# Kernel tuning notes

Hardware: AMD Instinct MI355X
Metric: run time of the kernel (lower is better)

## Reference

```python
import jax, jax.numpy as jnp
import numpy as np

NEG_SLOPE = 0.2


def _gat_layer(x, src, dst, W, a_src, a_dst, b, concat):
    """PyG-style GATConv (with self-loops already appended to src/dst).
    x: [N, Fin], W: [Fin, H*D], a_src/a_dst: [H, D], b: [H*D] or [D].
    """
    N = x.shape[0]
    H, D = a_src.shape
    h = (x @ W).reshape(N, H, D)                      # per-head projections
    es = jnp.einsum('nhd,hd->nh', h, a_src)           # alpha_src per node
    ed = jnp.einsum('nhd,hd->nh', h, a_dst)           # alpha_dst per node
    e = jax.nn.leaky_relu(es[src] + ed[dst], NEG_SLOPE)   # [E, H] edge logits
    # segment softmax over incoming edges of each target node
    m = jax.ops.segment_max(e, dst, num_segments=N)       # [N, H]
    ex = jnp.exp(e - m[dst])
    s = jax.ops.segment_sum(ex, dst, num_segments=N)      # [N, H]
    alpha = ex / jnp.where(s > 0, s, 1.0)[dst]            # [E, H]
    out = jax.ops.segment_sum(h[src] * alpha[:, :, None], dst, num_segments=N)  # [N,H,D]
    out = out.reshape(N, H * D) if concat else out.mean(axis=1)
    return out + b


def setup_inputs() -> dict:
    key = jax.random.key(0)
    ks = jax.random.split(key, 16)
    N, E, F_IN, HID, HEADS, NG, NC = 50000, 1000000, 128, 64, 4, 512, 2
    x = jax.random.normal(ks[0], (N, F_IN), dtype=jnp.float32)
    edge_index = jax.random.randint(ks[1], (2, E), 0, N, dtype=jnp.int32)
    batch = jnp.sort(jax.random.randint(ks[2], (N,), 0, NG, dtype=jnp.int32))
    sc = 0.1
    params = {
        'W1': jax.random.normal(ks[3], (F_IN, HEADS * HID), dtype=jnp.float32) * sc,
        'a_src1': jax.random.normal(ks[4], (HEADS, HID), dtype=jnp.float32) * sc,
        'a_dst1': jax.random.normal(ks[5], (HEADS, HID), dtype=jnp.float32) * sc,
        'b1': jnp.zeros((HEADS * HID,), dtype=jnp.float32),
        'W2': jax.random.normal(ks[6], (HEADS * HID, HID), dtype=jnp.float32) * sc,
        'a_src2': jax.random.normal(ks[7], (1, HID), dtype=jnp.float32) * sc,
        'a_dst2': jax.random.normal(ks[8], (1, HID), dtype=jnp.float32) * sc,
        'b2': jnp.zeros((HID,), dtype=jnp.float32),
        'Wc': jax.random.normal(ks[9], (HID, NC), dtype=jnp.float32) * sc,
        'bc': jnp.zeros((NC,), dtype=jnp.float32),
    }
    return {'x': x, 'edge_index': edge_index, 'batch': batch, 'num_graphs': NG, **params}


def reference(x, edge_index, batch, num_graphs, W1, a_src1, a_dst1, b1,
              W2, a_src2, a_dst2, b2, Wc, bc):
    N = x.shape[0]
    # PyG GATConv adds self-loops by default
    loops = jnp.arange(N, dtype=edge_index.dtype)
    src = jnp.concatenate([edge_index[0], loops])
    dst = jnp.concatenate([edge_index[1], loops])
    h = jax.nn.elu(_gat_layer(x, src, dst, W1, a_src1, a_dst1, b1, concat=True))
    h = jax.nn.elu(_gat_layer(h, src, dst, W2, a_src2, a_dst2, b2, concat=False))
    # global mean pool per graph
    sums = jax.ops.segment_sum(h, batch, num_segments=num_graphs)         # [G, HID]
    cnt = jax.ops.segment_sum(jnp.ones((N,), h.dtype), batch, num_segments=num_graphs)
    pooled = sums / jnp.maximum(cnt, 1.0)[:, None]
    return pooled @ Wc + bc
```

## Files before the change

kernel.cpp:

```cpp
#include <hip/hip_runtime.h>

#define NN   50000
#define NE   1000000
#define FIN  128
#define HID  64
#define HEADS 4
#define C1   256
#define NG   512
#define ETOT (NE + NN)
#define BSH  10
#define NBUK 49
#define CHUNK 8192
#define NCHUNK 123
#define NPREP 192
#define NHIST 64

typedef __attribute__((ext_vector_type(8))) short bf16x8;
typedef __attribute__((ext_vector_type(4))) short bf16x4;
typedef __attribute__((ext_vector_type(4))) float f32x4;
typedef __attribute__((ext_vector_type(2))) float f32x2;

__device__ __forceinline__ float lrelu(float v) { return v > 0.f ? v : 0.2f * v; }
__device__ __forceinline__ float eluf(float v)  { return v > 0.f ? v : __expf(v) - 1.f; }

__device__ __forceinline__ unsigned short f2bf(float f) {
    unsigned u = __float_as_uint(f);
    unsigned r = (u + 0x7FFFu + ((u >> 16) & 1u)) >> 16;
    return (unsigned short)r;
}
__device__ __forceinline__ float bf2f(unsigned short b) {
    return __uint_as_float(((unsigned)b) << 16);
}
__device__ __forceinline__ unsigned char f2fp8(float f) {
    int w = __builtin_amdgcn_cvt_pk_fp8_f32(f, f, 0, false);
    return (unsigned char)(w & 0xFF);
}

__global__ __launch_bounds__(256) void k_setup(const float* __restrict__ W1,
                                               const float* __restrict__ W2,
                                               const int* __restrict__ dst,
                                               const int* __restrict__ batch,
                                               unsigned short* __restrict__ W1t,
                                               unsigned short* __restrict__ W2t,
                                               int* __restrict__ bhist,
                                               int* __restrict__ gstart) {
    int b = blockIdx.x;
    int tid = threadIdx.x;
    if (b < NPREP) {
        int i = b * 256 + tid;
        if (i < FIN * C1) {
            int k = i / C1, c = i % C1;
            W1t[c * FIN + k] = f2bf(W1[i]);
        } else {
            int j = i - FIN * C1;
            if (j < C1 * HID) {
                int k = j / HID, c = j % HID;
                W2t[c * C1 + k] = f2bf(W2[j]);
            }
        }
    } else if (b < NPREP + NHIST) {
        __shared__ int lh[NBUK];
        if (tid < NBUK) lh[tid] = 0;
        __syncthreads();
        for (int e = (b - NPREP) * 256 + tid; e < NE; e += NHIST * 256)
            atomicAdd(&lh[dst[e] >> BSH], 1);
        __syncthreads();
        if (tid < NBUK) atomicAdd(&bhist[tid], lh[tid]);
    } else {
        for (int g = tid; g <= NG; g += 256) {
            int lo = 0, hi = NN;
            while (lo < hi) {
                int mid = (lo + hi) >> 1;
                if (batch[mid] < g) lo = mid + 1; else hi = mid;
            }
            gstart[g] = lo;
        }
    }
}

__global__ void k_bscan(const int* __restrict__ bhist,
                        int* __restrict__ bbase,
                        int* __restrict__ bcur,
                        int* __restrict__ offs) {
    int tid = threadIdx.x;
    int v = (tid < NBUK) ? bhist[tid] : 0;
    int x = v;
    #pragma unroll
    for (int off = 1; off < 64; off <<= 1) {
        int t = __shfl_up(x, off);
        if (tid >= off) x += t;
    }
    if (tid < NBUK) {
        int excl = x - v;
        bbase[tid] = excl;
        bcur[tid] = excl;
    }
    if (tid == NBUK - 1) bbase[NBUK] = x;
    if (tid == 0) offs[NN] = ETOT;
}

__global__ __launch_bounds__(256) void k_part(const int* __restrict__ src,
                                              const int* __restrict__ dst,
                                              int* __restrict__ bcur,
                                              int2* __restrict__ ebuf) {
    __shared__ int lcnt[NBUK];
    __shared__ int gbase[NBUK];
    __shared__ int lrank[NBUK];
    int tid = threadIdx.x;
    int e0 = blockIdx.x * CHUNK;
    int e1 = min(e0 + CHUNK, NE);
    if (tid < NBUK) { lcnt[tid] = 0; lrank[tid] = 0; }
    __syncthreads();
    for (int e = e0 + tid; e < e1; e += 256)
        atomicAdd(&lcnt[dst[e] >> BSH], 1);
    __syncthreads();
    if (tid < NBUK) gbase[tid] = atomicAdd(&bcur[tid], lcnt[tid]);
    __syncthreads();
    for (int e = e0 + tid; e < e1; e += 256) {
        int d = dst[e];
        int b = d >> BSH;
        int r = atomicAdd(&lrank[b], 1);
        ebuf[gbase[b] + r] = make_int2(src[e], d);
    }
}

__global__ __launch_bounds__(1024) void k_bfill(const int2* __restrict__ ebuf,
                                                const int* __restrict__ bbase,
                                                int* __restrict__ offs,
                                                int* __restrict__ colsrc) {
    __shared__ int ldeg[1024];
    __shared__ int lcur[1024];
    __shared__ int ws[16];
    int b = blockIdx.x;
    int tid = threadIdx.x;
    int nbase = b << BSH;
    int ncnt = min(1024, NN - nbase);
    int ebeg = bbase[b], eend = bbase[b + 1];
    ldeg[tid] = 0;
    __syncthreads();
    for (int i = ebeg + tid; i < eend; i += 1024)
        atomicAdd(&ldeg[ebuf[i].y - nbase], 1);
    __syncthreads();
    int v = (tid < ncnt) ? ldeg[tid] + 1 : 0;
    int lane = tid & 63, wv = tid >> 6;
    int x = v;
    #pragma unroll
    for (int off = 1; off < 64; off <<= 1) {
        int t = __shfl_up(x, off);
        if (lane >= off) x += t;
    }
    if (lane == 63) ws[wv] = x;
    __syncthreads();
    if (tid < 16) {
        int y = ws[tid];
        #pragma unroll
        for (int off = 1; off < 16; off <<= 1) {
            int t = __shfl_up(y, off);
            if (tid >= off) y += t;
        }
        ws[tid] = y;
    }
    __syncthreads();
    int base = wv ? ws[wv - 1] : 0;
    int excl = base + x - v;
    int gofs = ebeg + nbase + excl;
    if (tid < ncnt) {
        offs[nbase + tid] = gofs;
        lcur[tid] = gofs;
    }
    __syncthreads();
    for (int i = ebeg + tid; i < eend; i += 1024) {
        int2 ed = ebuf[i];
        int p = atomicAdd(&lcur[ed.y - nbase], 1);
        colsrc[p] = ed.x;
    }
    __syncthreads();
    if (tid < ncnt) colsrc[lcur[tid]] = nbase + tid;
}

__global__ __launch_bounds__(256) void k_gemm1(const float* __restrict__ x,
                                               const unsigned short* __restrict__ W1t,
                                               const float* __restrict__ asrc,
                                               const float* __restrict__ adst,
                                               unsigned char* __restrict__ h1f,
                                               float* __restrict__ es1,
                                               float* __restrict__ ed1) {
    __shared__ unsigned short Wl[128 * FIN];
    int tid = threadIdx.x;
    int lane = tid & 63, wv = tid >> 6;
    int r0 = (blockIdx.x * 4 + wv) * 16;
    int g = lane >> 4, q = lane & 15;

    int ar = min(r0 + q, NN - 1);
    const float* xr = x + (size_t)ar * FIN;
    bf16x8 afr[4];
    #pragma unroll
    for (int kt = 0; kt < 4; ++kt) {
        float4 u0 = *(const float4*)(xr + kt * 32 + g * 8);
        float4 u1 = *(const float4*)(xr + kt * 32 + g * 8 + 4);
        bf16x8 a;
        a[0] = (short)f2bf(u0.x); a[1] = (short)f2bf(u0.y);
        a[2] = (short)f2bf(u0.z); a[3] = (short)f2bf(u0.w);
        a[4] = (short)f2bf(u1.x); a[5] = (short)f2bf(u1.y);
        a[6] = (short)f2bf(u1.z); a[7] = (short)f2bf(u1.w);
        afr[kt] = a;
    }

    for (int ch = 0; ch < 2; ++ch) {
        if (ch) __syncthreads();
        const uint4* src = (const uint4*)(W1t + (size_t)ch * 128 * FIN);
        #pragma unroll
        for (int i = 0; i < 8; ++i) {
            int idx = tid + i * 256;
            uint4 v = src[idx];
            unsigned byte = (unsigned)idx << 4;
            unsigned dst = byte ^ (((byte >> 8) & 7) << 4);
            *(uint4*)((char*)Wl + dst) = v;
        }
        __syncthreads();

        #pragma unroll
        for (int hh = 0; hh < 2; ++hh) {
            int h = ch * 2 + hh;
            float ps[4] = {0.f, 0.f, 0.f, 0.f};
            float pd[4] = {0.f, 0.f, 0.f, 0.f};
            #pragma unroll
            for (int tl = 0; tl < 4; ++tl) {
                int col = (h * 4 + tl) * 16 + q;
                int cl = col - ch * 128;
                f32x4 acc = {0.f, 0.f, 0.f, 0.f};
                #pragma unroll
                for (int kt = 0; kt < 4; ++kt) {
                    unsigned bb = (unsigned)cl * 256 + kt * 64 + g * 16;
                    bf16x8 b = *(const bf16x8*)((const char*)Wl + (bb ^ (((unsigned)cl & 7) << 4)));
                    acc = __builtin_amdgcn_mfma_f32_16x16x32_bf16(afr[kt], b, acc, 0, 0, 0);
                }
                float av = asrc[col], bv = adst[col];
                #pragma unroll
                for (int j = 0; j < 4; ++j) {
                    int rr = min(r0 + g * 4 + j, NN - 1);
                    h1f[(size_t)rr * C1 + col] = f2fp8(acc[j]);
                    ps[j] += acc[j] * av;
                    pd[j] += acc[j] * bv;
                }
            }
            #pragma unroll
            for (int j = 0; j < 4; ++j) {
                #pragma unroll
                for (int off = 1; off < 16; off <<= 1) {
                    ps[j] += __shfl_xor(ps[j], off);
                    pd[j] += __shfl_xor(pd[j], off);
                }
                if (q == 0) {
                    int rr = min(r0 + g * 4 + j, NN - 1);
                    es1[rr * 4 + h] = ps[j];
                    ed1[rr * 4 + h] = pd[j];
                }
            }
        }
    }
}

__global__ __launch_bounds__(512) void k_agg1(const int* __restrict__ offs,
                                              const int* __restrict__ colsrc,
                                              const unsigned char* __restrict__ h1f,
                                              const float* __restrict__ es1,
                                              const float* __restrict__ ed1,
                                              const float* __restrict__ b1,
                                              unsigned short* __restrict__ h1p) {
    __shared__ int   sls[8][64];
    __shared__ float sla[8][64][4];
    int lane = threadIdx.x & 63, wv = threadIdx.x >> 6;
    int n = blockIdx.x * 8 + wv;
    if (n >= NN) return;
    int beg = offs[n], end = offs[n + 1], deg = end - beg;
    float4 edv = *(const float4*)(ed1 + n * 4);
    int half = lane >> 5, q5 = lane & 31;
    int hd = q5 >> 3;
    f32x2 acc2[4];
    #pragma unroll
    for (int j = 0; j < 4; ++j) acc2[j] = (f32x2){0.f, 0.f};

    if (deg <= 64) {
        int msrc = 0;
        float m0 = 0.f, m1 = 0.f, m2 = 0.f, m3 = 0.f;
        if (lane < deg) {
            msrc = colsrc[beg + lane];
            float4 ev = *(const float4*)(es1 + msrc * 4);
            m0 = __expf(lrelu(ev.x + edv.x));
            m1 = __expf(lrelu(ev.y + edv.y));
            m2 = __expf(lrelu(ev.z + edv.z));
            m3 = __expf(lrelu(ev.w + edv.w));
        }
        float s0 = m0, s1 = m1, s2 = m2, s3 = m3;
        #pragma unroll
        for (int off = 1; off < 64; off <<= 1) {
            s0 += __shfl_xor(s0, off);
            s1 += __shfl_xor(s1, off);
            s2 += __shfl_xor(s2, off);
            s3 += __shfl_xor(s3, off);
        }
        sls[wv][lane] = msrc;
        sla[wv][lane][0] = m0 * (1.f / s0);
        sla[wv][lane][1] = m1 * (1.f / s1);
        sla[wv][lane][2] = m2 * (1.f / s2);
        sla[wv][lane][3] = m3 * (1.f / s3);

        for (int i = 0; i < deg; i += 16) {
            uint2 hv[8];
            float a[8];
            #pragma unroll
            for (int u = 0; u < 8; ++u) {
                int ee = (i + 2 * u + half) & 63;
                int s = sls[wv][ee];
                a[u] = sla[wv][ee][hd];
                hv[u] = *(const uint2*)(h1f + (size_t)s * C1 + q5 * 8);
            }
            #pragma unroll
            for (int u = 0; u < 8; ++u) {
                f32x2 av = (f32x2){a[u], a[u]};
                f32x2 p;
                p = __builtin_amdgcn_cvt_pk_f32_fp8(hv[u].x, false); acc2[0] += p * av;
                p = __builtin_amdgcn_cvt_pk_f32_fp8(hv[u].x, true);  acc2[1] += p * av;
                p = __builtin_amdgcn_cvt_pk_f32_fp8(hv[u].y, false); acc2[2] += p * av;
                p = __builtin_amdgcn_cvt_pk_f32_fp8(hv[u].y, true);  acc2[3] += p * av;
            }
        }
    } else {
        float s0 = 0.f, s1 = 0.f, s2 = 0.f, s3 = 0.f;
        for (int i = beg + lane; i < end; i += 64) {
            int s = colsrc[i];
            float4 ev = *(const float4*)(es1 + s * 4);
            s0 += __expf(lrelu(ev.x + edv.x));
            s1 += __expf(lrelu(ev.y + edv.y));
            s2 += __expf(lrelu(ev.z + edv.z));
            s3 += __expf(lrelu(ev.w + edv.w));
        }
        #pragma unroll
        for (int off = 1; off < 64; off <<= 1) {
            s0 += __shfl_xor(s0, off);
            s1 += __shfl_xor(s1, off);
            s2 += __shfl_xor(s2, off);
            s3 += __shfl_xor(s3, off);
        }
        float rr = hd == 0 ? 1.f / s0 : hd == 1 ? 1.f / s1 : hd == 2 ? 1.f / s2 : 1.f / s3;
        float ed_h = hd == 0 ? edv.x : hd == 1 ? edv.y : hd == 2 ? edv.z : edv.w;
        for (int i = beg; i < end; i += 2) {
            int idx = i + half;
            if (idx < end) {
                int s = colsrc[idx];
                float eh = es1[s * 4 + hd] + ed_h;
                float av = __expf(lrelu(eh)) * rr;
                f32x2 a = (f32x2){av, av};
                uint2 hv = *(const uint2*)(h1f + (size_t)s * C1 + q5 * 8);
                f32x2 p;
                p = __builtin_amdgcn_cvt_pk_f32_fp8(hv.x, false); acc2[0] += p * a;
                p = __builtin_amdgcn_cvt_pk_f32_fp8(hv.x, true);  acc2[1] += p * a;
                p = __builtin_amdgcn_cvt_pk_f32_fp8(hv.y, false); acc2[2] += p * a;
                p = __builtin_amdgcn_cvt_pk_f32_fp8(hv.y, true);  acc2[3] += p * a;
            }
        }
    }

    float acc[8];
    #pragma unroll
    for (int j = 0; j < 4; ++j) { acc[2*j] = acc2[j][0]; acc[2*j+1] = acc2[j][1]; }
    #pragma unroll
    for (int j = 0; j < 8; ++j) acc[j] += __shfl_xor(acc[j], 32);

    if (half == 0) {
        float4 bv0 = *(const float4*)(b1 + q5 * 8);
        float4 bv1 = *(const float4*)(b1 + q5 * 8 + 4);
        bf16x8 o;
        o[0] = (short)f2bf(eluf(acc[0] + bv0.x));
        o[1] = (short)f2bf(eluf(acc[1] + bv0.y));
        o[2] = (short)f2bf(eluf(acc[2] + bv0.z));
        o[3] = (short)f2bf(eluf(acc[3] + bv0.w));
        o[4] = (short)f2bf(eluf(acc[4] + bv1.x));
        o[5] = (short)f2bf(eluf(acc[5] + bv1.y));
        o[6] = (short)f2bf(eluf(acc[6] + bv1.z));
        o[7] = (short)f2bf(eluf(acc[7] + bv1.w));
        *(bf16x8*)(h1p + (size_t)n * C1 + q5 * 8) = o;
    }
}

__global__ __launch_bounds__(256) void k_gemm2(const unsigned short* __restrict__ h1p,
                                               const unsigned short* __restrict__ W2t,
                                               const float* __restrict__ as2,
                                               const float* __restrict__ ad2,
                                               unsigned char* __restrict__ h2f,
                                               float* __restrict__ es2,
                                               float* __restrict__ ed2) {
    __shared__ unsigned short Wl[HID * C1];
    int tid = threadIdx.x;
    int lane = tid & 63, wv = tid >> 6;
    int r0 = (blockIdx.x * 4 + wv) * 16;
    int g = lane >> 4, q = lane & 15;

    const uint4* src = (const uint4*)W2t;
    #pragma unroll
    for (int i = 0; i < 8; ++i) {
        int idx = tid + i * 256;
        uint4 v = src[idx];
        unsigned byte = (unsigned)idx << 4;
        unsigned dst = byte ^ (((byte >> 9) & 7) << 4);
        *(uint4*)((char*)Wl + dst) = v;
    }

    int ar = min(r0 + q, NN - 1);
    const unsigned short* arp = h1p + (size_t)ar * C1;
    bf16x8 afr[8];
    #pragma unroll
    for (int kt = 0; kt < 8; ++kt)
        afr[kt] = *(const bf16x8*)(arp + kt * 32 + g * 8);

    __syncthreads();

    float ps[4] = {0.f, 0.f, 0.f, 0.f};
    float pd[4] = {0.f, 0.f, 0.f, 0.f};
    #pragma unroll
    for (int t = 0; t < 4; ++t) {
        int col = t * 16 + q;
        f32x4 acc = {0.f, 0.f, 0.f, 0.f};
        #pragma unroll
        for (int kt = 0; kt < 8; ++kt) {
            unsigned bb = (unsigned)col * 512 + kt * 64 + g * 16;
            bf16x8 b = *(const bf16x8*)((const char*)Wl + (bb ^ (((unsigned)col & 7) << 4)));
            acc = __builtin_amdgcn_mfma_f32_16x16x32_bf16(afr[kt], b, acc, 0, 0, 0);
        }
        float av = as2[col], bv = ad2[col];
        #pragma unroll
        for (int j = 0; j < 4; ++j) {
            int rr = min(r0 + g * 4 + j, NN - 1);
            h2f[(size_t)rr * HID + col] = f2fp8(acc[j]);
            ps[j] += acc[j] * av;
            pd[j] += acc[j] * bv;
        }
    }
    #pragma unroll
    for (int j = 0; j < 4; ++j) {
        #pragma unroll
        for (int off = 1; off < 16; off <<= 1) {
            ps[j] += __shfl_xor(ps[j], off);
            pd[j] += __shfl_xor(pd[j], off);
        }
        if (q == 0) {
            int rr = min(r0 + g * 4 + j, NN - 1);
            es2[rr] = ps[j];
            ed2[rr] = pd[j];
        }
    }
}

__global__ __launch_bounds__(512) void k_agg2(const int* __restrict__ offs,
                                              const int* __restrict__ colsrc,
                                              const unsigned char* __restrict__ h2f,
                                              const float* __restrict__ es2,
                                              const float* __restrict__ ed2,
                                              const float* __restrict__ b2,
                                              float* __restrict__ h3) {
    __shared__ int   sls[8][64];
    __shared__ float sla[8][64];
    int lane = threadIdx.x & 63, wv = threadIdx.x >> 6;
    int n = blockIdx.x * 8 + wv;
    if (n >= NN) return;
    int beg = offs[n], end = offs[n + 1], deg = end - beg;
    float edv = ed2[n];
    int g = lane >> 4, q = lane & 15;
    f32x2 acc2[2];
    acc2[0] = (f32x2){0.f, 0.f};
    acc2[1] = (f32x2){0.f, 0.f};

    if (deg <= 64) {
        int msrc = 0;
        float mex = 0.f;
        if (lane < deg) {
            msrc = colsrc[beg + lane];
            mex = __expf(lrelu(es2[msrc] + edv));
        }
        float ss = mex;
        #pragma unroll
        for (int off = 1; off < 64; off <<= 1) ss += __shfl_xor(ss, off);
        sls[wv][lane] = msrc;
        sla[wv][lane] = mex * (1.f / ss);

        for (int i = 0; i < deg; i += 32) {
            unsigned w[8];
            float a[8];
            #pragma unroll
            for (int u = 0; u < 8; ++u) {
                int ee = (i + 4 * u + g) & 63;
                int s = sls[wv][ee];
                a[u] = sla[wv][ee];
                w[u] = *(const unsigned*)(h2f + (size_t)s * HID + q * 4);
            }
            #pragma unroll
            for (int u = 0; u < 8; ++u) {
                f32x2 av = (f32x2){a[u], a[u]};
                f32x2 p;
                p = __builtin_amdgcn_cvt_pk_f32_fp8(w[u], false); acc2[0] += p * av;
                p = __builtin_amdgcn_cvt_pk_f32_fp8(w[u], true);  acc2[1] += p * av;
            }
        }
    } else {
        float ss = 0.f;
        for (int i = beg + lane; i < end; i += 64) {
            int s = colsrc[i];
            ss += __expf(lrelu(es2[s] + edv));
        }
        #pragma unroll
        for (int off = 1; off < 64; off <<= 1) ss += __shfl_xor(ss, off);
        float rs = 1.f / ss;
        for (int i = beg; i < end; i += 4) {
            int idx = i + g;
            if (idx < end) {
                int s = colsrc[idx];
                float av = __expf(lrelu(es2[s] + edv)) * rs;
                f32x2 a = (f32x2){av, av};
                unsigned w = *(const unsigned*)(h2f + (size_t)s * HID + q * 4);
                f32x2 p;
                p = __builtin_amdgcn_cvt_pk_f32_fp8(w, false); acc2[0] += p * a;
                p = __builtin_amdgcn_cvt_pk_f32_fp8(w, true);  acc2[1] += p * a;
            }
        }
    }

    float acc[4] = {acc2[0][0], acc2[0][1], acc2[1][0], acc2[1][1]};
    #pragma unroll
    for (int j = 0; j < 4; ++j) {
        acc[j] += __shfl_xor(acc[j], 16);
        acc[j] += __shfl_xor(acc[j], 32);
    }

    float v0 = __shfl(acc[0], lane >> 2);
    float v1 = __shfl(acc[1], lane >> 2);
    float v2 = __shfl(acc[2], lane >> 2);
    float v3 = __shfl(acc[3], lane >> 2);
    int jj = lane & 3;
    float o = jj == 0 ? v0 : jj == 1 ? v1 : jj == 2 ? v2 : v3;
    h3[(size_t)n * HID + lane] = eluf(o + b2[lane]);
}

__global__ __launch_bounds__(256) void k_poolcls(const float* __restrict__ h3,
                                                 const int* __restrict__ gstart,
                                                 const float* __restrict__ Wc,
                                                 const float* __restrict__ bc,
                                                 float* __restrict__ out) {
    __shared__ float red[4][64];
    int g = blockIdx.x;
    int lane = threadIdx.x & 63, wv = threadIdx.x >> 6;
    int gs = gstart[g], ge = gstart[g + 1];
    float acc = 0.f;
    for (int r = gs + wv; r < ge; r += 4)
        acc += h3[(size_t)r * HID + lane];
    red[wv][lane] = acc;
    __syncthreads();
    if (wv == 0) {
        float p = red[0][lane] + red[1][lane] + red[2][lane] + red[3][lane];
        float c = fmaxf((float)(ge - gs), 1.f);
        p /= c;
        float s0 = p * Wc[lane * 2 + 0];
        float s1 = p * Wc[lane * 2 + 1];
        #pragma unroll
        for (int off = 1; off < 64; off <<= 1) {
            s0 += __shfl_xor(s0, off);
            s1 += __shfl_xor(s1, off);
        }
        if (lane == 0) {
            out[g * 2 + 0] = s0 + bc[0];
            out[g * 2 + 1] = s1 + bc[1];
        }
    }
}

extern "C" void kernel_launch(void* const* d_in, const int* in_sizes, int n_in,
                              void* d_out, int out_size, void* d_ws, size_t ws_size,
                              hipStream_t stream) {
    const float* x   = (const float*)d_in[0];
    const int* ei    = (const int*)d_in[1];
    const int* batch = (const int*)d_in[2];
    const float* W1  = (const float*)d_in[4];
    const float* as1 = (const float*)d_in[5];
    const float* ad1 = (const float*)d_in[6];
    const float* b1  = (const float*)d_in[7];
    const float* W2  = (const float*)d_in[8];
    const float* as2 = (const float*)d_in[9];
    const float* ad2 = (const float*)d_in[10];
    const float* b2  = (const float*)d_in[11];
    const float* Wc  = (const float*)d_in[12];
    const float* bc  = (const float*)d_in[13];
    float* out = (float*)d_out;

    char* p = (char*)d_ws;
    auto alloc = [&](size_t bytes) -> char* {
        char* r = p;
        p += (bytes + 255) & ~(size_t)255;
        return r;
    };
    int* offs    = (int*)alloc((NN + 1) * sizeof(int));
    int* colsrc  = (int*)alloc((size_t)ETOT * sizeof(int));
    int2* ebuf   = (int2*)alloc((size_t)NE * sizeof(int2));
    int* bhist   = (int*)alloc(NBUK * sizeof(int));
    int* bbase   = (int*)alloc((NBUK + 1) * sizeof(int));
    int* bcur    = (int*)alloc(NBUK * sizeof(int));
    int* gstart  = (int*)alloc((NG + 1) * sizeof(int));
    unsigned short* W1t = (unsigned short*)alloc((size_t)FIN * C1 * sizeof(short));
    unsigned short* W2t = (unsigned short*)alloc((size_t)C1 * HID * sizeof(short));
    unsigned char* h1f  = (unsigned char*)alloc((size_t)NN * C1);
    unsigned short* h1p = (unsigned short*)alloc((size_t)NN * C1 * sizeof(short));
    unsigned char* h2f  = (unsigned char*)alloc((size_t)NN * HID);
    float* es1   = (float*)alloc((size_t)NN * 4 * sizeof(float));
    float* ed1   = (float*)alloc((size_t)NN * 4 * sizeof(float));
    float* es2v  = (float*)alloc((size_t)NN * sizeof(float));
    float* ed2v  = (float*)alloc((size_t)NN * sizeof(float));
    float* h3    = (float*)alloc((size_t)NN * HID * sizeof(float));

    hipMemsetAsync(bhist, 0, NBUK * sizeof(int), stream);

    const int* srcA = ei;
    const int* dstA = ei + NE;

    k_setup<<<NPREP + NHIST + 1, 256, 0, stream>>>(W1, W2, dstA, batch, W1t, W2t, bhist, gstart);
    k_bscan<<<1, 64, 0, stream>>>(bhist, bbase, bcur, offs);
    k_part<<<NCHUNK, 256, 0, stream>>>(srcA, dstA, bcur, ebuf);
    k_bfill<<<NBUK, 1024, 0, stream>>>(ebuf, bbase, offs, colsrc);

    k_gemm1<<<(NN / 16 + 3) / 4, 256, 0, stream>>>(x, W1t, as1, ad1, h1f, es1, ed1);
    k_agg1<<<(NN + 7) / 8, 512, 0, stream>>>(offs, colsrc, h1f, es1, ed1, b1, h1p);
    k_gemm2<<<(NN / 16 + 3) / 4, 256, 0, stream>>>(h1p, W2t, as2, ad2, h2f, es2v, ed2v);
    k_agg2<<<(NN + 7) / 8, 512, 0, stream>>>(offs, colsrc, h2f, es2v, ed2v, b2, h3);
    k_poolcls<<<NG, 256, 0, stream>>>(h3, gstart, Wc, bc, out);
}
```

Baseline: 193.8 us.

## Pack partitioned edges into one int and software-pipeline aggregation gathers

The bucket-partition buffer now stores each edge as a single 32-bit word, with the local destination in the upper 15 bits and the source in the lower 17, instead of an int2. This halves the traffic of that intermediate buffer. Both GAT aggregation loops for low-degree nodes are restructured into a double-buffered loop of 4 loads per step, prefetching the next group while the current one is converted and accumulated. The per-iteration batch drops from 8 to 4, which lowers memory-level parallelism per step and adds register copies, in exchange for overlapping loads with compute.

Result: faster. 187.1 us (-3.5%).

```diff
diff --git a/kernel.cpp b/kernel.cpp
--- a/kernel.cpp
+++ b/kernel.cpp
@@ -102,7 +102,7 @@
 __global__ __launch_bounds__(256) void k_part(const int* __restrict__ src,
                                               const int* __restrict__ dst,
                                               int* __restrict__ bcur,
-                                              int2* __restrict__ ebuf) {
+                                              int* __restrict__ ebuf) {
     __shared__ int lcnt[NBUK];
     __shared__ int gbase[NBUK];
     __shared__ int lrank[NBUK];
@@ -120,11 +120,11 @@
         int d = dst[e];
         int b = d >> BSH;
         int r = atomicAdd(&lrank[b], 1);
-        ebuf[gbase[b] + r] = make_int2(src[e], d);
-    }
-}
-
-__global__ __launch_bounds__(1024) void k_bfill(const int2* __restrict__ ebuf,
+        ebuf[gbase[b] + r] = ((d & 1023) << 17) | src[e];
+    }
+}
+
+__global__ __launch_bounds__(1024) void k_bfill(const int* __restrict__ ebuf,
                                                 const int* __restrict__ bbase,
                                                 int* __restrict__ offs,
                                                 int* __restrict__ colsrc) {
@@ -139,7 +139,7 @@
     ldeg[tid] = 0;
     __syncthreads();
     for (int i = ebeg + tid; i < eend; i += 1024)
-        atomicAdd(&ldeg[ebuf[i].y - nbase], 1);
+        atomicAdd(&ldeg[ebuf[i] >> 17], 1);
     __syncthreads();
     int v = (tid < ncnt) ? ldeg[tid] + 1 : 0;
     int lane = tid & 63, wv = tid >> 6;
@@ -170,9 +170,9 @@
     }
     __syncthreads();
     for (int i = ebeg + tid; i < eend; i += 1024) {
-        int2 ed = ebuf[i];
-        int p = atomicAdd(&lcur[ed.y - nbase], 1);
-        colsrc[p] = ed.x;
+        int pe = ebuf[i];
+        int p = atomicAdd(&lcur[pe >> 17], 1);
+        colsrc[p] = pe & 0x1FFFF;
     }
     __syncthreads();
     if (tid < ncnt) colsrc[lcur[tid]] = nbase + tid;
@@ -306,18 +306,23 @@
         sla[wv][lane][2] = m2 * (1.f / s2);
         sla[wv][lane][3] = m3 * (1.f / s3);
 
-        for (int i = 0; i < deg; i += 16) {
-            uint2 hv[8];
-            float a[8];
-            #pragma unroll
-            for (int u = 0; u < 8; ++u) {
-                int ee = (i + 2 * u + half) & 63;
+        auto ld4 = [&](int base, uint2* dhv, float* da) {
+            #pragma unroll
+            for (int u = 0; u < 4; ++u) {
+                int ee = (base + 2 * u + half) & 63;
                 int s = sls[wv][ee];
-                a[u] = sla[wv][ee][hd];
-                hv[u] = *(const uint2*)(h1f + (size_t)s * C1 + q5 * 8);
-            }
-            #pragma unroll
-            for (int u = 0; u < 8; ++u) {
+                da[u] = sla[wv][ee][hd];
+                dhv[u] = *(const uint2*)(h1f + (size_t)s * C1 + q5 * 8);
+            }
+        };
+        int iters = (deg + 7) >> 3;
+        uint2 hv[4]; float a[4];
+        uint2 nhv[4] = {}; float na[4] = {};
+        ld4(0, hv, a);
+        for (int it = 0; it < iters; ++it) {
+            if (it + 1 < iters) ld4((it + 1) * 8, nhv, na);
+            #pragma unroll
+            for (int u = 0; u < 4; ++u) {
                 f32x2 av = (f32x2){a[u], a[u]};
                 f32x2 p;
                 p = __builtin_amdgcn_cvt_pk_f32_fp8(hv[u].x, false); acc2[0] += p * av;
@@ -325,6 +330,8 @@
                 p = __builtin_amdgcn_cvt_pk_f32_fp8(hv[u].y, false); acc2[2] += p * av;
                 p = __builtin_amdgcn_cvt_pk_f32_fp8(hv[u].y, true);  acc2[3] += p * av;
             }
+            #pragma unroll
+            for (int u = 0; u < 4; ++u) { hv[u] = nhv[u]; a[u] = na[u]; }
         }
     } else {
         float s0 = 0.f, s1 = 0.f, s2 = 0.f, s3 = 0.f;
@@ -484,23 +491,30 @@
         sls[wv][lane] = msrc;
         sla[wv][lane] = mex * (1.f / ss);
 
-        for (int i = 0; i < deg; i += 32) {
-            unsigned w[8];
-            float a[8];
-            #pragma unroll
-            for (int u = 0; u < 8; ++u) {
-                int ee = (i + 4 * u + g) & 63;
+        auto ld4 = [&](int base, unsigned* dw, float* da) {
+            #pragma unroll
+            for (int u = 0; u < 4; ++u) {
+                int ee = (base + 4 * u + g) & 63;
                 int s = sls[wv][ee];
-                a[u] = sla[wv][ee];
-                w[u] = *(const unsigned*)(h2f + (size_t)s * HID + q * 4);
-            }
-            #pragma unroll
-            for (int u = 0; u < 8; ++u) {
+                da[u] = sla[wv][ee];
+                dw[u] = *(const unsigned*)(h2f + (size_t)s * HID + q * 4);
+            }
+        };
+        int iters = (deg + 15) >> 4;
+        unsigned w[4]; float a[4];
+        unsigned nw[4] = {}; float na[4] = {};
+        ld4(0, w, a);
+        for (int it = 0; it < iters; ++it) {
+            if (it + 1 < iters) ld4((it + 1) * 16, nw, na);
+            #pragma unroll
+            for (int u = 0; u < 4; ++u) {
                 f32x2 av = (f32x2){a[u], a[u]};
                 f32x2 p;
                 p = __builtin_amdgcn_cvt_pk_f32_fp8(w[u], false); acc2[0] += p * av;
                 p = __builtin_amdgcn_cvt_pk_f32_fp8(w[u], true);  acc2[1] += p * av;
             }
+            #pragma unroll
+            for (int u = 0; u < 4; ++u) { w[u] = nw[u]; a[u] = na[u]; }
         }
     } else {
         float ss = 0.f;
@@ -599,7 +613,7 @@
     };
     int* offs    = (int*)alloc((NN + 1) * sizeof(int));
     int* colsrc  = (int*)alloc((size_t)ETOT * sizeof(int));
-    int2* ebuf   = (int2*)alloc((size_t)NE * sizeof(int2));
+    int* ebuf    = (int*)alloc((size_t)NE * sizeof(int));
     int* bhist   = (int*)alloc(NBUK * sizeof(int));
     int* bbase   = (int*)alloc((NBUK + 1) * sizeof(int));
     int* bcur    = (int*)alloc(NBUK * sizeof(int));
```
